# Kernel optimization log

Hardware: AMD Instinct MI355X
Metric: run time of the kernel (lower is better)

Reference implementation:

```python
import jax, jax.numpy as jnp
import numpy as np
import math

B, S, HID, H = 4, 1024, 1024, 16
DH = HID // H

def setup_inputs() -> dict:
    key = jax.random.key(0)
    ks = jax.random.split(key, 16)
    inp = {
        'q': jax.random.normal(ks[0], (B, S, HID), jnp.float32),
        'k': jax.random.normal(ks[1], (B, S, HID), jnp.float32),
        'v': jax.random.normal(ks[2], (B, S, HID), jnp.float32),
        'k_b': jax.random.normal(ks[3], (B, S, HID), jnp.float32),
        'mask': jax.random.randint(ks[4], (B, S), 0, 2, jnp.int32),
    }
    sc = 1.0 / math.sqrt(HID)
    names = ['Wq', 'Wk', 'Wv', 'Wkb', 'Wo']
    for i, n in enumerate(names):
        inp[n] = jax.random.normal(ks[5 + i], (HID, HID), jnp.float32) * sc
        inp['b' + n[1:]] = jnp.zeros((HID,), jnp.float32)
    return inp

def _split_heads(x):
    # [B,S,HID] -> [B,H,S,DH]
    return x.reshape(B, S, H, DH).transpose(0, 2, 1, 3)

def reference(q, k, v, k_b, mask, Wq, bq, Wk, bk, Wv, bv, Wkb, bkb, Wo, bo):
    qh = _split_heads(q @ Wq.T + bq)
    kh = _split_heads(k @ Wk.T + bk)
    vh = _split_heads(v @ Wv.T + bv)
    kbh = _split_heads(k_b @ Wkb.T + bkb)
    scale = 1.0 / math.sqrt(3 * DH)
    # Q@K^T + Q@Kb^T == Q@(K+Kb)^T
    corr = jnp.einsum('bhsd,bhtd->bhst', qh, kh + kbh) * scale
    # mask[b,j] broadcast over heads and query positions
    corr = jnp.where(mask[:, None, None, :] == 0, jnp.float32(-1e9), corr)
    prob = jax.nn.softmax(corr, axis=-1)  # dropout p=0 (eval)
    hidden = jnp.einsum('bhst,bhtd->bhsd', prob, vh)
    hidden = hidden.transpose(0, 2, 1, 3).reshape(B, S, HID)
    return hidden @ Wo.T + bo
```

## Files before the change

kernel.cpp:

```cpp
#include <hip/hip_runtime.h>
#include <hip/hip_bf16.h>
#include <stdint.h>

#define B_   4
#define S_   1024
#define HID_ 1024
#define H_   16
#define DH_  64

typedef short bf16x8 __attribute__((ext_vector_type(8)));
typedef float f32x4  __attribute__((ext_vector_type(4)));
typedef unsigned int u32;
typedef unsigned short u16;

typedef u32 __attribute__((address_space(1))) as1_u32;
typedef u32 __attribute__((address_space(3))) as3_u32;

__device__ __forceinline__ f32x4 mfma16(bf16x8 a, bf16x8 b, f32x4 c) {
  return __builtin_amdgcn_mfma_f32_16x16x32_bf16(a, b, c, 0, 0, 0);
}

__device__ __forceinline__ void gload16(const void* g, void* l) {
  __builtin_amdgcn_global_load_lds((const as1_u32*)g, (as3_u32*)l, 16, 0, 0);
}

__device__ __forceinline__ u16 f2bf(float f) {
  __hip_bfloat16 h = __float2bfloat16(f);
  union { __hip_bfloat16 h; u16 u; } cv; cv.h = h; return cv.u;
}

__device__ __forceinline__ u32 cvtpk(float lo, float hi) {
  u32 r;
  asm("v_cvt_pk_bf16_f32 %0, %1, %2" : "=v"(r) : "v"(lo), "v"(hi));
  return r;
}

template<int NC>
__device__ __forceinline__ void stage_tile(const u16* __restrict__ src, char* smem, int bo,
                                           int tid, int w) {
  #pragma unroll
  for (int is = 0; is < NC; ++is) {
    int o = is * 4096 + tid * 16;
    int row = o >> 7, ch = (o >> 4) & 7;
    gload16(src + (size_t)row * HID_ + ((ch ^ (row & 7)) * 8),
            smem + bo + is * 4096 + w * 1024);
  }
}

__global__ __launch_bounds__(256) void cvt_all(
    const float* a0, const float* a1, const float* a2, const float* a3,
    const float* w0, const float* w1, const float* w2, const float* w3, const float* w4,
    u16* da0, u16* da1, u16* da2, u16* da3,
    u16* dw0, u16* dw1, u16* dw2, u16* dw3, u16* dw4) {
  int bb = blockIdx.x;
  const float* s; u16* d; size_t i;
  if (bb < 8192) {
    int t = bb * 256 + threadIdx.x;
    int sel = t >> 19;
    i = (size_t)(t & 524287) * 8;
    if (sel == 0)      { s = a0; d = da0; }
    else if (sel == 1) { s = a1; d = da1; }
    else if (sel == 2) { s = a2; d = da2; }
    else               { s = a3; d = da3; }
  } else {
    int t = (bb - 8192) * 256 + threadIdx.x;
    int sel = t >> 17;
    i = (size_t)(t & 131071) * 8;
    if (sel == 0)      { s = w0; d = dw0; }
    else if (sel == 1) { s = w1; d = dw1; }
    else if (sel == 2) { s = w2; d = dw2; }
    else if (sel == 3) { s = w3; d = dw3; }
    else               { s = w4; d = dw4; }
  }
  float4 v0 = *(const float4*)(s + i);
  float4 v1 = *(const float4*)(s + i + 4);
  uint4 r;
  r.x = cvtpk(v0.x, v0.y);
  r.y = cvtpk(v0.z, v0.w);
  r.z = cvtpk(v1.x, v1.y);
  r.w = cvtpk(v1.z, v1.w);
  *(uint4*)(d + i) = r;
}

__global__ __launch_bounds__(256) void gemm_proj(
    const u16* __restrict__ qbf, const u16* __restrict__ Wqbf,
    const u16* __restrict__ kbf, const u16* __restrict__ Wkbf,
    const u16* __restrict__ kbbf, const u16* __restrict__ Wkbbf,
    const u16* __restrict__ vbf, const u16* __restrict__ Wvbf,
    const float* __restrict__ bq, const float* __restrict__ bk,
    const float* __restrict__ bkb, const float* __restrict__ bv,
    u16* __restrict__ Qp, u16* __restrict__ KKp, u16* __restrict__ Vtp) {
  __shared__ __align__(16) char smem[65536];
  const int tid = threadIdx.x;
  const int lane = tid & 63, w = tid >> 6;
  const int g = lane >> 4, ql = lane & 15;
  const int wm = w >> 1, wn = w & 1;
  const int xr = ql & 7;
  const int xcd = blockIdx.x & 7, idx = blockIdx.x >> 3;

  if (idx < 64) {
    const int kkid = xcd * 64 + idx;
    const int m0 = (kkid >> 4) * 128;
    const int n0 = (kkid & 15) * 64;
    f32x4 acc[4][2];
    #pragma unroll
    for (int mi = 0; mi < 4; ++mi)
      #pragma unroll
      for (int ni = 0; ni < 2; ++ni) acc[mi][ni] = f32x4{0.f, 0.f, 0.f, 0.f};

    stage_tile<4>(kbf + (size_t)m0 * HID_, smem, 0, tid, w);
    stage_tile<2>(Wkbf + (size_t)n0 * HID_, smem, 16384, tid, w);

    #pragma unroll 1
    for (int kt = 0; kt < 32; ++kt) {
      const int boA = (kt & 1) ? 32768 : 0;
      const int boW = (kt & 1) ? 49152 : 16384;
      if (kt < 31) {
        int kn = kt + 1;
        const u16* As = (kn < 16) ? kbf : kbbf;
        const u16* Ws = (kn < 16) ? Wkbf : Wkbbf;
        int kk = (kn & 15) * 64;
        stage_tile<4>(As + (size_t)m0 * HID_ + kk, smem, boA ^ 32768, tid, w);
        stage_tile<2>(Ws + (size_t)n0 * HID_ + kk, smem, boW ^ (16384 ^ 49152), tid, w);
        asm volatile("s_waitcnt vmcnt(6)" ::: "memory");
      } else {
        asm volatile("s_waitcnt vmcnt(0)" ::: "memory");
      }
      __builtin_amdgcn_s_barrier();
      const char* ab = smem + boA;
      const char* wb = smem + boW;
      bf16x8 af[4][2], bfv[2][2];
      #pragma unroll
      for (int mi = 0; mi < 4; ++mi)
        #pragma unroll
        for (int c = 0; c < 2; ++c) {
          int row = wm * 64 + mi * 16 + ql;
          af[mi][c] = *(const bf16x8*)(ab + row * 128 + (((c * 4 + g) ^ xr) * 16));
        }
      #pragma unroll
      for (int ni = 0; ni < 2; ++ni)
        #pragma unroll
        for (int c = 0; c < 2; ++c) {
          int row = wn * 32 + ni * 16 + ql;
          bfv[ni][c] = *(const bf16x8*)(wb + row * 128 + (((c * 4 + g) ^ xr) * 16));
        }
      __builtin_amdgcn_s_setprio(1);
      #pragma unroll
      for (int c = 0; c < 2; ++c)
        #pragma unroll
        for (int mi = 0; mi < 4; ++mi)
          #pragma unroll
          for (int ni = 0; ni < 2; ++ni)
            acc[mi][ni] = mfma16(af[mi][c], bfv[ni][c], acc[mi][ni]);
      __builtin_amdgcn_s_setprio(0);
      __builtin_amdgcn_s_barrier();
    }
    #pragma unroll
    for (int ni = 0; ni < 2; ++ni) {
      int n = n0 + wn * 32 + ni * 16 + ql;
      float bs = bk[n] + bkb[n];
      #pragma unroll
      for (int mi = 0; mi < 4; ++mi)
        #pragma unroll
        for (int i = 0; i < 4; ++i) {
          int m = m0 + wm * 64 + mi * 16 + g * 4 + i;
          KKp[(size_t)m * HID_ + n] = f2bf(acc[mi][ni][i] + bs);
        }
    }
    return;
  }

  const int unit = (idx < 96) ? 0 : 1;
  const int uid = xcd * 32 + (idx & 31);
  const int m0 = (uid >> 3) * 128;
  const int n0 = (uid & 7) * 128;
  const u16* A0 = unit ? vbf : qbf;
  const u16* W0 = unit ? Wvbf : Wqbf;
  const float* b0 = unit ? bv : bq;
  const float osc = unit ? 1.f : 0.07216878364870322f * 1.44269504088896340f;

  f32x4 acc[4][4];
  #pragma unroll
  for (int mi = 0; mi < 4; ++mi)
    #pragma unroll
    for (int ni = 0; ni < 4; ++ni) acc[mi][ni] = f32x4{0.f, 0.f, 0.f, 0.f};

  stage_tile<4>(A0 + (size_t)m0 * HID_, smem, 0, tid, w);
  stage_tile<4>(W0 + (size_t)n0 * HID_, smem, 16384, tid, w);

  #pragma unroll 1
  for (int kt = 0; kt < 16; ++kt) {
    const int boA = (kt & 1) ? 32768 : 0;
    const int boW = (kt & 1) ? 49152 : 16384;
    if (kt < 15) {
      int kk = (kt + 1) * 64;
      stage_tile<4>(A0 + (size_t)m0 * HID_ + kk, smem, boA ^ 32768, tid, w);
      stage_tile<4>(W0 + (size_t)n0 * HID_ + kk, smem, boW ^ (16384 ^ 49152), tid, w);
      asm volatile("s_waitcnt vmcnt(8)" ::: "memory");
    } else {
      asm volatile("s_waitcnt vmcnt(0)" ::: "memory");
    }
    __builtin_amdgcn_s_barrier();
    const char* ab = smem + boA;
    const char* wb = smem + boW;
    bf16x8 af[4][2], bfv[4][2];
    #pragma unroll
    for (int mi = 0; mi < 4; ++mi)
      #pragma unroll
      for (int c = 0; c < 2; ++c) {
        int row = wm * 64 + mi * 16 + ql;
        af[mi][c] = *(const bf16x8*)(ab + row * 128 + (((c * 4 + g) ^ xr) * 16));
      }
    #pragma unroll
    for (int ni = 0; ni < 4; ++ni)
      #pragma unroll
      for (int c = 0; c < 2; ++c) {
        int row = wn * 64 + ni * 16 + ql;
        bfv[ni][c] = *(const bf16x8*)(wb + row * 128 + (((c * 4 + g) ^ xr) * 16));
      }
    __builtin_amdgcn_s_setprio(1);
    #pragma unroll
    for (int c = 0; c < 2; ++c)
      #pragma unroll
      for (int mi = 0; mi < 4; ++mi)
        #pragma unroll
        for (int ni = 0; ni < 4; ++ni)
          acc[mi][ni] = mfma16(af[mi][c], bfv[ni][c], acc[mi][ni]);
    __builtin_amdgcn_s_setprio(0);
    __builtin_amdgcn_s_barrier();
  }

  if (unit == 0) {
    #pragma unroll
    for (int ni = 0; ni < 4; ++ni) {
      int n = n0 + wn * 64 + ni * 16 + ql;
      float bs = b0[n];
      #pragma unroll
      for (int mi = 0; mi < 4; ++mi)
        #pragma unroll
        for (int i = 0; i < 4; ++i) {
          int m = m0 + wm * 64 + mi * 16 + g * 4 + i;
          Qp[(size_t)m * HID_ + n] = f2bf((acc[mi][ni][i] + bs) * osc);
        }
    }
  } else {
    char* tp = smem + w * 8192;
    #pragma unroll
    for (int ni = 0; ni < 4; ++ni) {
      int n = n0 + wn * 64 + ni * 16 + ql;
      float bs = b0[n];
      #pragma unroll
      for (int mi = 0; mi < 4; ++mi)
        #pragma unroll
        for (int i = 0; i < 4; ++i) {
          int nl = ni * 16 + ql;
          int ml = mi * 16 + g * 4 + i;
          *(u16*)(tp + nl * 128 + (((ml >> 3) ^ (nl & 7)) * 16) + (ml & 7) * 2) =
              f2bf(acc[mi][ni][i] + bs);
        }
    }
    __syncthreads();
    int nl = lane;
    int n = n0 + wn * 64 + nl;
    int h = n >> 6, dh = n & 63;
    int mb = m0 + wm * 64;
    int b = mb >> 10, s0 = mb & 1023;
    int bh = b * H_ + h;
    u16* orow = Vtp + (((size_t)(bh * DH_ + dh)) << 10) + s0;
    #pragma unroll
    for (int j = 0; j < 8; ++j) {
      uint4 val = *(const uint4*)(tp + nl * 128 + ((j ^ (nl & 7)) * 16));
      *(uint4*)(orow + j * 8) = val;
    }
  }
}

__global__ __launch_bounds__(256) void gemm_o(const u16* __restrict__ A0, const u16* __restrict__ W0,
                                              const float* __restrict__ bias0, float* __restrict__ outp) {
  __shared__ __align__(16) char smem[49152];
  const int tid = threadIdx.x;
  const int lane = tid & 63, w = tid >> 6;
  const int g = lane >> 4, ql = lane & 15;
  const int wm = w >> 1, wn = w & 1;
  const int logical = (blockIdx.x & 7) * 64 + (blockIdx.x >> 3);
  const int m0 = (logical >> 4) * 128;
  const int n0 = (logical & 15) * 64;
  const int xr = ql & 7;

  f32x4 acc[4][2];
  #pragma unroll
  for (int mi = 0; mi < 4; ++mi)
    #pragma unroll
    for (int ni = 0; ni < 2; ++ni) acc[mi][ni] = f32x4{0.f, 0.f, 0.f, 0.f};

  stage_tile<4>(A0 + (size_t)m0 * HID_, smem, 0, tid, w);
  stage_tile<2>(W0 + (size_t)n0 * HID_, smem, 32768, tid, w);

  #pragma unroll 1
  for (int kt = 0; kt < 16; ++kt) {
    const int boA = (kt & 1) ? 16384 : 0;
    const int boW = (kt & 1) ? 40960 : 32768;
    if (kt < 15) {
      int kk = (kt + 1) * 64;
      stage_tile<4>(A0 + (size_t)m0 * HID_ + kk, smem, boA ^ 16384, tid, w);
      stage_tile<2>(W0 + (size_t)n0 * HID_ + kk, smem, boW ^ (32768 ^ 40960), tid, w);
      asm volatile("s_waitcnt vmcnt(6)" ::: "memory");
    } else {
      asm volatile("s_waitcnt vmcnt(0)" ::: "memory");
    }
    __builtin_amdgcn_s_barrier();
    const char* ab = smem + boA;
    const char* wb = smem + boW;
    bf16x8 af[4][2], bfv[2][2];
    #pragma unroll
    for (int mi = 0; mi < 4; ++mi)
      #pragma unroll
      for (int c = 0; c < 2; ++c) {
        int row = wm * 64 + mi * 16 + ql;
        af[mi][c] = *(const bf16x8*)(ab + row * 128 + (((c * 4 + g) ^ xr) * 16));
      }
    #pragma unroll
    for (int ni = 0; ni < 2; ++ni)
      #pragma unroll
      for (int c = 0; c < 2; ++c) {
        int row = wn * 32 + ni * 16 + ql;
        bfv[ni][c] = *(const bf16x8*)(wb + row * 128 + (((c * 4 + g) ^ xr) * 16));
      }
    __builtin_amdgcn_s_setprio(1);
    #pragma unroll
    for (int c = 0; c < 2; ++c)
      #pragma unroll
      for (int mi = 0; mi < 4; ++mi)
        #pragma unroll
        for (int ni = 0; ni < 2; ++ni)
          acc[mi][ni] = mfma16(af[mi][c], bfv[ni][c], acc[mi][ni]);
    __builtin_amdgcn_s_setprio(0);
    __builtin_amdgcn_s_barrier();
  }

  #pragma unroll
  for (int ni = 0; ni < 2; ++ni) {
    int n = n0 + wn * 32 + ni * 16 + ql;
    float bs = bias0[n];
    #pragma unroll
    for (int mi = 0; mi < 4; ++mi)
      #pragma unroll
      for (int i = 0; i < 4; ++i) {
        int m = m0 + wm * 64 + mi * 16 + g * 4 + i;
        outp[(size_t)m * HID_ + n] = acc[mi][ni][i] + bs;
      }
  }
}

__global__ __launch_bounds__(256, 4) void attn(const u16* __restrict__ Qp, const u16* __restrict__ KKp,
                                               const u16* __restrict__ Vt, const int* __restrict__ mask,
                                               u16* __restrict__ hidden) {
  __shared__ __align__(16) char smem[40960];
  const int tid = threadIdx.x;
  const int lane = tid & 63, w = tid >> 6;
  const int g = lane >> 4, ql = lane & 15;
  const int bid = blockIdx.x;
  const int bh = (bid & 7) * 8 + ((bid >> 3) & 7);
  const int qt = bid >> 6;
  const int b = bh >> 4, h = bh & 15;
  const int q0 = qt * 64;
  const int xr = ql & 7;

  #pragma unroll
  for (int is = 0; is < 2; ++is) {
    int o = is * 4096 + tid * 16;
    int row = o >> 7, ch = (o >> 4) & 7;
    gload16(KKp + (size_t)(b * S_ + row) * HID_ + h * DH_ + ((ch ^ (row & 7)) * 8),
            smem + is * 4096 + w * 1024);
    gload16(Vt + (size_t)(bh * DH_ + row) * S_ + ((ch ^ (row & 7)) * 8),
            smem + 8192 + is * 4096 + w * 1024);
  }

  const u16* qrow = Qp + (size_t)(b * S_ + q0 + w * 16 + ql) * HID_ + h * DH_;
  bf16x8 qb0 = *(const bf16x8*)(qrow + g * 8);
  bf16x8 qb1 = *(const bf16x8*)(qrow + 32 + g * 8);
  const int* maskp = mask + b * S_;

  f32x4 oacc[4];
  #pragma unroll
  for (int d = 0; d < 4; ++d) oacc[d] = f32x4{0.f, 0.f, 0.f, 0.f};
  float m_run = -1e30f, l_run = 0.f;
  char* pbase = smem + 32768 + w * 2048 + ql * 128;

  int pb = 0;
  for (int it = 0; it < 16; ++it) {
    const int k0 = it * 64;
    int4 mv[4];
    #pragma unroll
    for (int t = 0; t < 4; ++t) mv[t] = *(const int4*)(maskp + k0 + 16 * t + 4 * g);
    __builtin_amdgcn_sched_barrier(0);
    if (it < 15) {
      const int k0s = k0 + 64;
      const int bo = (pb ^ 1) * 16384;
      #pragma unroll
      for (int is = 0; is < 2; ++is) {
        int o = is * 4096 + tid * 16;
        int row = o >> 7, ch = (o >> 4) & 7;
        gload16(KKp + (size_t)(b * S_ + k0s + row) * HID_ + h * DH_ + ((ch ^ (row & 7)) * 8),
                smem + bo + is * 4096 + w * 1024);
        gload16(Vt + (size_t)(bh * DH_ + row) * S_ + k0s + ((ch ^ (row & 7)) * 8),
                smem + bo + 8192 + is * 4096 + w * 1024);
      }
      asm volatile("s_waitcnt vmcnt(4)" ::: "memory");
    } else {
      asm volatile("s_waitcnt vmcnt(0)" ::: "memory");
    }
    __builtin_amdgcn_s_barrier();

    const char* kb_ = smem + pb * 16384;
    const char* vb_ = smem + pb * 16384 + 8192;

    float sv[4][4];
    #pragma unroll
    for (int t = 0; t < 4; ++t) {
      const char* krow = kb_ + (16 * t + ql) * 128;
      bf16x8 ka0 = *(const bf16x8*)(krow + ((g ^ xr) * 16));
      bf16x8 ka1 = *(const bf16x8*)(krow + (((4 + g) ^ xr) * 16));
      f32x4 st = mfma16(ka0, qb0, f32x4{0.f, 0.f, 0.f, 0.f});
      st = mfma16(ka1, qb1, st);
      sv[t][0] = mv[t].x ? st[0] : -1e9f;
      sv[t][1] = mv[t].y ? st[1] : -1e9f;
      sv[t][2] = mv[t].z ? st[2] : -1e9f;
      sv[t][3] = mv[t].w ? st[3] : -1e9f;
    }
    float mloc = sv[0][0];
    #pragma unroll
    for (int t = 0; t < 4; ++t)
      #pragma unroll
      for (int i = 0; i < 4; ++i) mloc = fmaxf(mloc, sv[t][i]);
    mloc = fmaxf(mloc, __shfl_xor(mloc, 16, 64));
    mloc = fmaxf(mloc, __shfl_xor(mloc, 32, 64));
    if (__any(mloc > m_run + 10.f)) {
      float mnew = fmaxf(m_run, mloc);
      float alpha = __builtin_amdgcn_exp2f(m_run - mnew);
      l_run *= alpha;
      #pragma unroll
      for (int d = 0; d < 4; ++d) oacc[d] *= alpha;
      m_run = mnew;
    }
    float rsum = 0.f;
    float pvs[4][4];
    #pragma unroll
    for (int t = 0; t < 4; ++t)
      #pragma unroll
      for (int i = 0; i < 4; ++i) {
        float p = __builtin_amdgcn_exp2f(sv[t][i] - m_run);
        pvs[t][i] = p; rsum += p;
      }
    rsum += __shfl_xor(rsum, 16, 64);
    rsum += __shfl_xor(rsum, 32, 64);
    l_run += rsum;

    #pragma unroll
    for (int t = 0; t < 4; ++t) {
      uint2 pw;
      pw.x = cvtpk(pvs[t][0], pvs[t][1]);
      pw.y = cvtpk(pvs[t][2], pvs[t][3]);
      *(uint2*)(pbase + (((4 * t + g) ^ (2 * xr)) * 8)) = pw;
    }
    #pragma unroll
    for (int c = 0; c < 2; ++c) {
      bf16x8 pf = *(const bf16x8*)(pbase + (((c * 4 + g) ^ xr) * 16));
      #pragma unroll
      for (int d = 0; d < 4; ++d) {
        bf16x8 va = *(const bf16x8*)(vb_ + (16 * d + ql) * 128 + (((c * 4 + g) ^ xr) * 16));
        oacc[d] = mfma16(va, pf, oacc[d]);
      }
    }
    __builtin_amdgcn_s_barrier();
    pb ^= 1;
  }

  float inv = 1.0f / l_run;
  char* ep = smem + w * 2304;
  #pragma unroll
  for (int d = 0; d < 4; ++d)
    #pragma unroll
    for (int i = 0; i < 4; ++i)
      *(u16*)(ep + ql * 144 + (16 * d + 4 * g + i) * 2) = f2bf(oacc[d][i] * inv);
  __syncthreads();
  int r = lane >> 2, cc = lane & 3;
  const char* erow = smem + w * 2304 + r * 144 + cc * 32;
  uint4 v0 = *(const uint4*)erow;
  uint4 v1 = *(const uint4*)(erow + 16);
  u16* orow = hidden + (size_t)(b * S_ + q0 + w * 16 + r) * HID_ + h * DH_ + cc * 16;
  *(uint4*)orow = v0;
  *(uint4*)(orow + 8) = v1;
}

extern "C" void kernel_launch(void* const* d_in, const int* in_sizes, int n_in,
                              void* d_out, int out_size, void* d_ws, size_t ws_size,
                              hipStream_t stream) {
  (void)in_sizes; (void)n_in; (void)out_size; (void)ws_size;
  const float* q    = (const float*)d_in[0];
  const float* k    = (const float*)d_in[1];
  const float* v    = (const float*)d_in[2];
  const float* kb   = (const float*)d_in[3];
  const int*   mask = (const int*)  d_in[4];
  const float* Wq   = (const float*)d_in[5];
  const float* bq   = (const float*)d_in[6];
  const float* Wk   = (const float*)d_in[7];
  const float* bk   = (const float*)d_in[8];
  const float* Wv   = (const float*)d_in[9];
  const float* bv   = (const float*)d_in[10];
  const float* Wkb  = (const float*)d_in[11];
  const float* bkb  = (const float*)d_in[12];
  const float* Wo   = (const float*)d_in[13];
  const float* bo   = (const float*)d_in[14];

  char* ws = (char*)d_ws;
  const size_t MB = 1024 * 1024;
  u16* qbf   = (u16*)(ws + 0 * MB);
  u16* kbf   = (u16*)(ws + 8 * MB);
  u16* vbf   = (u16*)(ws + 16 * MB);
  u16* kbbf  = (u16*)(ws + 24 * MB);
  u16* Wqbf  = (u16*)(ws + 32 * MB);
  u16* Wkbf  = (u16*)(ws + 34 * MB);
  u16* Wvbf  = (u16*)(ws + 36 * MB);
  u16* Wkbbf = (u16*)(ws + 38 * MB);
  u16* Wobf  = (u16*)(ws + 40 * MB);
  u16* Qp    = (u16*)(ws + 42 * MB);
  u16* KKp   = (u16*)(ws + 50 * MB);
  u16* Vtp   = (u16*)(ws + 58 * MB);
  u16* hid   = (u16*)(ws + 66 * MB);

  cvt_all<<<10752, 256, 0, stream>>>(q, k, v, kb, Wq, Wk, Wv, Wkb, Wo,
                                     qbf, kbf, vbf, kbbf, Wqbf, Wkbf, Wvbf, Wkbbf, Wobf);
  gemm_proj<<<1024, 256, 0, stream>>>(qbf, Wqbf, kbf, Wkbf, kbbf, Wkbbf, vbf, Wvbf,
                                      bq, bk, bkb, bv, Qp, KKp, Vtp);
  attn<<<1024, 256, 0, stream>>>(Qp, KKp, Vtp, mask, hid);
  gemm_o<<<512, 256, 0, stream>>>(hid, Wobf, bo, (float*)d_out);
}
```

Before: 123.1 us.

## Unify projection GEMM tiles to 128x64 and shrink LDS for 3 blocks per CU

```diff
diff --git a/kernel.cpp b/kernel.cpp
--- a/kernel.cpp
+++ b/kernel.cpp
@@ -82,7 +82,7 @@
   *(uint4*)(d + i) = r;
 }
 
-__global__ __launch_bounds__(256) void gemm_proj(
+__global__ __launch_bounds__(256, 3) void gemm_proj(
     const u16* __restrict__ qbf, const u16* __restrict__ Wqbf,
     const u16* __restrict__ kbf, const u16* __restrict__ Wkbf,
     const u16* __restrict__ kbbf, const u16* __restrict__ Wkbbf,
@@ -90,165 +90,99 @@
     const float* __restrict__ bq, const float* __restrict__ bk,
     const float* __restrict__ bkb, const float* __restrict__ bv,
     u16* __restrict__ Qp, u16* __restrict__ KKp, u16* __restrict__ Vtp) {
-  __shared__ __align__(16) char smem[65536];
+  __shared__ __align__(16) char smem[49152];
   const int tid = threadIdx.x;
   const int lane = tid & 63, w = tid >> 6;
   const int g = lane >> 4, ql = lane & 15;
   const int wm = w >> 1, wn = w & 1;
   const int xr = ql & 7;
   const int xcd = blockIdx.x & 7, idx = blockIdx.x >> 3;
-
-  if (idx < 64) {
-    const int kkid = xcd * 64 + idx;
-    const int m0 = (kkid >> 4) * 128;
-    const int n0 = (kkid & 15) * 64;
-    f32x4 acc[4][2];
+  const int unit = (idx < 64) ? 0 : (idx < 128) ? 1 : 2;
+  const int id = xcd * 64 + (idx & 63);
+  const int m0 = (id >> 4) * 128;
+  const int n0 = (id & 15) * 64;
+
+  const u16 *A0, *W0, *A1, *W1;
+  int nkt;
+  if (unit == 0)      { A0 = kbf; W0 = Wkbf; A1 = kbbf; W1 = Wkbbf; nkt = 32; }
+  else if (unit == 1) { A0 = qbf; W0 = Wqbf; A1 = qbf;  W1 = Wqbf;  nkt = 16; }
+  else                { A0 = vbf; W0 = Wvbf; A1 = vbf;  W1 = Wvbf;  nkt = 16; }
+
+  f32x4 acc[4][2];
+  #pragma unroll
+  for (int mi = 0; mi < 4; ++mi)
+    #pragma unroll
+    for (int ni = 0; ni < 2; ++ni) acc[mi][ni] = f32x4{0.f, 0.f, 0.f, 0.f};
+
+  stage_tile<4>(A0 + (size_t)m0 * HID_, smem, 0, tid, w);
+  stage_tile<2>(W0 + (size_t)n0 * HID_, smem, 16384, tid, w);
+
+  #pragma unroll 1
+  for (int kt = 0; kt < nkt; ++kt) {
+    const int boA = (kt & 1) ? 24576 : 0;
+    const int boW = (kt & 1) ? 40960 : 16384;
+    if (kt < nkt - 1) {
+      int kn = kt + 1;
+      const u16* As = (kn < 16) ? A0 : A1;
+      const u16* Ws = (kn < 16) ? W0 : W1;
+      int kk = (kn & 15) * 64;
+      stage_tile<4>(As + (size_t)m0 * HID_ + kk, smem, boA ^ 24576, tid, w);
+      stage_tile<2>(Ws + (size_t)n0 * HID_ + kk, smem, boW ^ (16384 ^ 40960), tid, w);
+      asm volatile("s_waitcnt vmcnt(6)" ::: "memory");
+    } else {
+      asm volatile("s_waitcnt vmcnt(0)" ::: "memory");
+    }
+    __builtin_amdgcn_s_barrier();
+    const char* ab = smem + boA;
+    const char* wb = smem + boW;
+    bf16x8 af[4][2], bfv[2][2];
     #pragma unroll
     for (int mi = 0; mi < 4; ++mi)
       #pragma unroll
-      for (int ni = 0; ni < 2; ++ni) acc[mi][ni] = f32x4{0.f, 0.f, 0.f, 0.f};
-
-    stage_tile<4>(kbf + (size_t)m0 * HID_, smem, 0, tid, w);
-    stage_tile<2>(Wkbf + (size_t)n0 * HID_, smem, 16384, tid, w);
-
-    #pragma unroll 1
-    for (int kt = 0; kt < 32; ++kt) {
-      const int boA = (kt & 1) ? 32768 : 0;
-      const int boW = (kt & 1) ? 49152 : 16384;
-      if (kt < 31) {
-        int kn = kt + 1;
-        const u16* As = (kn < 16) ? kbf : kbbf;
-        const u16* Ws = (kn < 16) ? Wkbf : Wkbbf;
-        int kk = (kn & 15) * 64;
-        stage_tile<4>(As + (size_t)m0 * HID_ + kk, smem, boA ^ 32768, tid, w);
-        stage_tile<2>(Ws + (size_t)n0 * HID_ + kk, smem, boW ^ (16384 ^ 49152), tid, w);
-        asm volatile("s_waitcnt vmcnt(6)" ::: "memory");
-      } else {
-        asm volatile("s_waitcnt vmcnt(0)" ::: "memory");
-      }
-      __builtin_amdgcn_s_barrier();
-      const char* ab = smem + boA;
-      const char* wb = smem + boW;
-      bf16x8 af[4][2], bfv[2][2];
+      for (int c = 0; c < 2; ++c) {
+        int row = wm * 64 + mi * 16 + ql;
+        af[mi][c] = *(const bf16x8*)(ab + row * 128 + (((c * 4 + g) ^ xr) * 16));
+      }
+    #pragma unroll
+    for (int ni = 0; ni < 2; ++ni)
+      #pragma unroll
+      for (int c = 0; c < 2; ++c) {
+        int row = wn * 32 + ni * 16 + ql;
+        bfv[ni][c] = *(const bf16x8*)(wb + row * 128 + (((c * 4 + g) ^ xr) * 16));
+      }
+    __builtin_amdgcn_s_setprio(1);
+    #pragma unroll
+    for (int c = 0; c < 2; ++c)
       #pragma unroll
       for (int mi = 0; mi < 4; ++mi)
         #pragma unroll
-        for (int c = 0; c < 2; ++c) {
-          int row = wm * 64 + mi * 16 + ql;
-          af[mi][c] = *(const bf16x8*)(ab + row * 128 + (((c * 4 + g) ^ xr) * 16));
-        }
-      #pragma unroll
-      for (int ni = 0; ni < 2; ++ni)
-        #pragma unroll
-        for (int c = 0; c < 2; ++c) {
-          int row = wn * 32 + ni * 16 + ql;
-          bfv[ni][c] = *(const bf16x8*)(wb + row * 128 + (((c * 4 + g) ^ xr) * 16));
-        }
-      __builtin_amdgcn_s_setprio(1);
-      #pragma unroll
-      for (int c = 0; c < 2; ++c)
-        #pragma unroll
-        for (int mi = 0; mi < 4; ++mi)
-          #pragma unroll
-          for (int ni = 0; ni < 2; ++ni)
-            acc[mi][ni] = mfma16(af[mi][c], bfv[ni][c], acc[mi][ni]);
-      __builtin_amdgcn_s_setprio(0);
-      __builtin_amdgcn_s_barrier();
-    }
+        for (int ni = 0; ni < 2; ++ni)
+          acc[mi][ni] = mfma16(af[mi][c], bfv[ni][c], acc[mi][ni]);
+    __builtin_amdgcn_s_setprio(0);
+    __builtin_amdgcn_s_barrier();
+  }
+
+  if (unit != 2) {
+    u16* outp = (unit == 0) ? KKp : Qp;
+    const float osc = (unit == 1) ? 0.07216878364870322f * 1.44269504088896340f : 1.f;
     #pragma unroll
     for (int ni = 0; ni < 2; ++ni) {
       int n = n0 + wn * 32 + ni * 16 + ql;
-      float bs = bk[n] + bkb[n];
+      float bs = (unit == 0) ? (bk[n] + bkb[n]) : bq[n];
       #pragma unroll
       for (int mi = 0; mi < 4; ++mi)
         #pragma unroll
         for (int i = 0; i < 4; ++i) {
           int m = m0 + wm * 64 + mi * 16 + g * 4 + i;
-          KKp[(size_t)m * HID_ + n] = f2bf(acc[mi][ni][i] + bs);
+          outp[(size_t)m * HID_ + n] = f2bf((acc[mi][ni][i] + bs) * osc);
         }
     }
-    return;
-  }
-
-  const int unit = (idx < 96) ? 0 : 1;
-  const int uid = xcd * 32 + (idx & 31);
-  const int m0 = (uid >> 3) * 128;
-  const int n0 = (uid & 7) * 128;
-  const u16* A0 = unit ? vbf : qbf;
-  const u16* W0 = unit ? Wvbf : Wqbf;
-  const float* b0 = unit ? bv : bq;
-  const float osc = unit ? 1.f : 0.07216878364870322f * 1.44269504088896340f;
-
-  f32x4 acc[4][4];
-  #pragma unroll
-  for (int mi = 0; mi < 4; ++mi)
-    #pragma unroll
-    for (int ni = 0; ni < 4; ++ni) acc[mi][ni] = f32x4{0.f, 0.f, 0.f, 0.f};
-
-  stage_tile<4>(A0 + (size_t)m0 * HID_, smem, 0, tid, w);
-  stage_tile<4>(W0 + (size_t)n0 * HID_, smem, 16384, tid, w);
-
-  #pragma unroll 1
-  for (int kt = 0; kt < 16; ++kt) {
-    const int boA = (kt & 1) ? 32768 : 0;
-    const int boW = (kt & 1) ? 49152 : 16384;
-    if (kt < 15) {
-      int kk = (kt + 1) * 64;
-      stage_tile<4>(A0 + (size_t)m0 * HID_ + kk, smem, boA ^ 32768, tid, w);
-      stage_tile<4>(W0 + (size_t)n0 * HID_ + kk, smem, boW ^ (16384 ^ 49152), tid, w);
-      asm volatile("s_waitcnt vmcnt(8)" ::: "memory");
-    } else {
-      asm volatile("s_waitcnt vmcnt(0)" ::: "memory");
-    }
-    __builtin_amdgcn_s_barrier();
-    const char* ab = smem + boA;
-    const char* wb = smem + boW;
-    bf16x8 af[4][2], bfv[4][2];
-    #pragma unroll
-    for (int mi = 0; mi < 4; ++mi)
-      #pragma unroll
-      for (int c = 0; c < 2; ++c) {
-        int row = wm * 64 + mi * 16 + ql;
-        af[mi][c] = *(const bf16x8*)(ab + row * 128 + (((c * 4 + g) ^ xr) * 16));
-      }
-    #pragma unroll
-    for (int ni = 0; ni < 4; ++ni)
-      #pragma unroll
-      for (int c = 0; c < 2; ++c) {
-        int row = wn * 64 + ni * 16 + ql;
-        bfv[ni][c] = *(const bf16x8*)(wb + row * 128 + (((c * 4 + g) ^ xr) * 16));
-      }
-    __builtin_amdgcn_s_setprio(1);
-    #pragma unroll
-    for (int c = 0; c < 2; ++c)
-      #pragma unroll
-      for (int mi = 0; mi < 4; ++mi)
-        #pragma unroll
-        for (int ni = 0; ni < 4; ++ni)
-          acc[mi][ni] = mfma16(af[mi][c], bfv[ni][c], acc[mi][ni]);
-    __builtin_amdgcn_s_setprio(0);
-    __builtin_amdgcn_s_barrier();
-  }
-
-  if (unit == 0) {
-    #pragma unroll
-    for (int ni = 0; ni < 4; ++ni) {
-      int n = n0 + wn * 64 + ni * 16 + ql;
-      float bs = b0[n];
-      #pragma unroll
-      for (int mi = 0; mi < 4; ++mi)
-        #pragma unroll
-        for (int i = 0; i < 4; ++i) {
-          int m = m0 + wm * 64 + mi * 16 + g * 4 + i;
-          Qp[(size_t)m * HID_ + n] = f2bf((acc[mi][ni][i] + bs) * osc);
-        }
-    }
   } else {
-    char* tp = smem + w * 8192;
-    #pragma unroll
-    for (int ni = 0; ni < 4; ++ni) {
-      int n = n0 + wn * 64 + ni * 16 + ql;
-      float bs = b0[n];
+    char* tp = smem + w * 4096;
+    #pragma unroll
+    for (int ni = 0; ni < 2; ++ni) {
+      int n = n0 + wn * 32 + ni * 16 + ql;
+      float bs = bv[n];
       #pragma unroll
       for (int mi = 0; mi < 4; ++mi)
         #pragma unroll
@@ -260,23 +194,22 @@
         }
     }
     __syncthreads();
-    int nl = lane;
-    int n = n0 + wn * 64 + nl;
+    int r = lane >> 1, half = lane & 1;
+    int n = n0 + wn * 32 + r;
     int h = n >> 6, dh = n & 63;
-    int mb = m0 + wm * 64;
-    int b = mb >> 10, s0 = mb & 1023;
+    int b = m0 >> 10;
     int bh = b * H_ + h;
-    u16* orow = Vtp + (((size_t)(bh * DH_ + dh)) << 10) + s0;
-    #pragma unroll
-    for (int j = 0; j < 8; ++j) {
-      uint4 val = *(const uint4*)(tp + nl * 128 + ((j ^ (nl & 7)) * 16));
+    u16* orow = Vtp + (((size_t)(bh * DH_ + dh)) << 10) + (m0 & 1023) + wm * 64 + half * 32;
+    #pragma unroll
+    for (int j = 0; j < 4; ++j) {
+      uint4 val = *(const uint4*)(tp + r * 128 + (((half * 4 + j) ^ (r & 7)) * 16));
       *(uint4*)(orow + j * 8) = val;
     }
   }
 }
 
-__global__ __launch_bounds__(256) void gemm_o(const u16* __restrict__ A0, const u16* __restrict__ W0,
-                                              const float* __restrict__ bias0, float* __restrict__ outp) {
+__global__ __launch_bounds__(256, 3) void gemm_o(const u16* __restrict__ A0, const u16* __restrict__ W0,
+                                                 const float* __restrict__ bias0, float* __restrict__ outp) {
   __shared__ __align__(16) char smem[49152];
   const int tid = threadIdx.x;
   const int lane = tid & 63, w = tid >> 6;
@@ -294,16 +227,16 @@
     for (int ni = 0; ni < 2; ++ni) acc[mi][ni] = f32x4{0.f, 0.f, 0.f, 0.f};
 
   stage_tile<4>(A0 + (size_t)m0 * HID_, smem, 0, tid, w);
-  stage_tile<2>(W0 + (size_t)n0 * HID_, smem, 32768, tid, w);
+  stage_tile<2>(W0 + (size_t)n0 * HID_, smem, 16384, tid, w);
 
   #pragma unroll 1
   for (int kt = 0; kt < 16; ++kt) {
-    const int boA = (kt & 1) ? 16384 : 0;
-    const int boW = (kt & 1) ? 40960 : 32768;
+    const int boA = (kt & 1) ? 24576 : 0;
+    const int boW = (kt & 1) ? 40960 : 16384;
     if (kt < 15) {
       int kk = (kt + 1) * 64;
-      stage_tile<4>(A0 + (size_t)m0 * HID_ + kk, smem, boA ^ 16384, tid, w);
-      stage_tile<2>(W0 + (size_t)n0 * HID_ + kk, smem, boW ^ (32768 ^ 40960), tid, w);
+      stage_tile<4>(A0 + (size_t)m0 * HID_ + kk, smem, boA ^ 24576, tid, w);
+      stage_tile<2>(W0 + (size_t)n0 * HID_ + kk, smem, boW ^ (16384 ^ 40960), tid, w);
       asm volatile("s_waitcnt vmcnt(6)" ::: "memory");
     } else {
       asm volatile("s_waitcnt vmcnt(0)" ::: "memory");
@@ -531,7 +464,7 @@
 
   cvt_all<<<10752, 256, 0, stream>>>(q, k, v, kb, Wq, Wk, Wv, Wkb, Wo,
                                      qbf, kbf, vbf, kbbf, Wqbf, Wkbf, Wvbf, Wkbbf, Wobf);
-  gemm_proj<<<1024, 256, 0, stream>>>(qbf, Wqbf, kbf, Wkbf, kbbf, Wkbbf, vbf, Wvbf,
+  gemm_proj<<<1536, 256, 0, stream>>>(qbf, Wqbf, kbf, Wkbf, kbbf, Wkbbf, vbf, Wvbf,
                                       bq, bk, bkb, bv, Qp, KKp, Vtp);
   attn<<<1024, 256, 0, stream>>>(Qp, KKp, Vtp, mask, hid);
   gemm_o<<<512, 256, 0, stream>>>(hid, Wobf, bo, (float*)d_out);
```

Result: faster. 119.8 us (-2.7%).
